# Kernel optimization log

Measured on AMD Instinct MI355X. Metric: run time of the kernel, lower is better.

## Reference

```python
import jax, jax.numpy as jnp
import numpy as np

B, S, IN, E, H, NH = 32, 1024, 16, 128, 256, 4
DH = E // NH
EPS = 1e-5


def _ln(x, g, b):
    mu = jnp.mean(x, axis=-1, keepdims=True)
    var = jnp.mean(jnp.square(x - mu), axis=-1, keepdims=True)
    return (x - mu) * jax.lax.rsqrt(var + EPS) * g + b


def setup_inputs() -> dict:
    key = jax.random.key(0)
    ks = iter(jax.random.split(key, 32))
    n = lambda shape, s=0.02: jax.random.normal(next(ks), shape, jnp.float32) * s
    inp = {
        "x": jax.random.normal(next(ks), (B, S, IN), jnp.float32),
        "mask": jax.random.uniform(next(ks), (B, S), jnp.float32),
        "embed_w": n((E, IN)), "embed_b": jnp.zeros((E,), jnp.float32),
        # 3 encoder layers, params stacked on leading layer axis
        "in_proj_w": n((3, 3 * E, E)), "in_proj_b": jnp.zeros((3, 3 * E), jnp.float32),
        "out_w": n((3, E, E)), "out_b": jnp.zeros((3, E), jnp.float32),
        "ln1_g": jnp.ones((3, E), jnp.float32), "ln1_b": jnp.zeros((3, E), jnp.float32),
        "ln2_g": jnp.ones((3, E), jnp.float32), "ln2_b": jnp.zeros((3, E), jnp.float32),
        "ffn_w1": n((3, E, E)), "ffn_b1": jnp.zeros((3, E), jnp.float32),
        "ffn_w2": n((3, E, E)), "ffn_b2": jnp.zeros((3, E), jnp.float32),
        "cls_w1": n((H, E)), "cls_b1": jnp.zeros((H,), jnp.float32),
        "cls_w2": n((H, H)), "cls_b2": jnp.zeros((H,), jnp.float32),
        "cls_w3": n((H, H)), "cls_b3": jnp.zeros((H,), jnp.float32),
        "cls_w4": n((1, H)), "cls_b4": jnp.zeros((1,), jnp.float32),
    }
    return inp


def _encoder_layer(x, ipw, ipb, ow, ob, g1, b1, g2, b2, w1, fb1, w2, fb2):
    # PyTorch TransformerEncoderLayer, norm_first=False (post-norm), relu FFN
    qkv = x @ ipw.T + ipb                      # [B,S,3E]
    q, k, v = jnp.split(qkv, 3, axis=-1)
    q = q.reshape(B, S, NH, DH).transpose(0, 2, 1, 3)
    k = k.reshape(B, S, NH, DH).transpose(0, 2, 1, 3)
    v = v.reshape(B, S, NH, DH).transpose(0, 2, 1, 3)
    scores = jnp.einsum("bhqd,bhkd->bhqk", q, k) / np.sqrt(DH)  # naive O(S^2) math SDPA
    attn = jax.nn.softmax(scores, axis=-1)
    o = jnp.einsum("bhqk,bhkd->bhqd", attn, v)
    o = o.transpose(0, 2, 1, 3).reshape(B, S, E) @ ow.T + ob
    x = _ln(x + o, g1, b1)
    ff = jax.nn.relu(x @ w1.T + fb1) @ w2.T + fb2
    return _ln(x + ff, g2, b2)


def reference(x, mask, embed_w, embed_b, in_proj_w, in_proj_b, out_w, out_b,
              ln1_g, ln1_b, ln2_g, ln2_b, ffn_w1, ffn_b1, ffn_w2, ffn_b2,
              cls_w1, cls_b1, cls_w2, cls_b2, cls_w3, cls_b3, cls_w4, cls_b4):
    h = jax.nn.relu(x @ embed_w.T + embed_b)   # [B,S,E]
    for i in range(3):
        h = _encoder_layer(h, in_proj_w[i], in_proj_b[i], out_w[i], out_b[i],
                           ln1_g[i], ln1_b[i], ln2_g[i], ln2_b[i],
                           ffn_w1[i], ffn_b1[i], ffn_w2[i], ffn_b2[i])
    pooled = jnp.sum(h * mask[:, :, None], axis=1)  # [B,E] masked sum pool
    z = jax.nn.relu(pooled @ cls_w1.T + cls_b1)
    z = jax.nn.relu(z @ cls_w2.T + cls_b2)
    z = jax.nn.relu(z @ cls_w3.T + cls_b3)
    return jax.nn.sigmoid(z @ cls_w4.T + cls_b4)    # [B,1]
```

## Files before the change

### kernel.cpp

```cpp
#include <hip/hip_runtime.h>
#include <hip/hip_bf16.h>
#include <math.h>

#define B 32
#define S 1024
#define IN_DIM 16
#define E 128
#define NH 4
#define DH 32
#define HDIM 256
#define ROWS (B*S)
#define EPS 1e-5f

#define N_IPW (3*384*128)
#define N_SQ  (3*128*128)

typedef __bf16 bf16x8 __attribute__((ext_vector_type(8)));
typedef __bf16 bf16x4 __attribute__((ext_vector_type(4)));
typedef __bf16 bf16x2 __attribute__((ext_vector_type(2)));
typedef float f32x4 __attribute__((ext_vector_type(4)));

union BF2U { bf16x2 b; unsigned int u; };
__device__ inline unsigned int pk2(float a, float b) {
    BF2U x; x.b[0] = (__bf16)a; x.b[1] = (__bf16)b; return x.u;
}

union U8 { bf16x8 v8; bf16x4 v4[2]; };
__device__ inline void st8(__bf16* p, bf16x8 v) {
    U8 u; u.v8 = v;
    *(bf16x4*)p = u.v4[0];
    *(bf16x4*)(p + 4) = u.v4[1];
}
__device__ inline bf16x8 ld8(const __bf16* p) {
    U8 u;
    u.v4[0] = *(const bf16x4*)p;
    u.v4[1] = *(const bf16x4*)(p + 4);
    return u.v8;
}

__global__ __launch_bounds__(256) void k_cvt(const float* __restrict__ ipw,
        const float* __restrict__ ow, const float* __restrict__ w1,
        const float* __restrict__ w2, __bf16* __restrict__ o)
{
    int i = blockIdx.x * 256 + threadIdx.x;
    float v;
    if (i < N_IPW) v = ipw[i];
    else if (i < N_IPW + N_SQ) v = ow[i - N_IPW];
    else if (i < N_IPW + 2 * N_SQ) v = w1[i - N_IPW - N_SQ];
    else v = w2[i - N_IPW - 2 * N_SQ];
    o[i] = (__bf16)v;
}

__global__ __launch_bounds__(128) void k_embed(const float* __restrict__ x,
        const float* __restrict__ W, const float* __restrict__ bias,
        __bf16* __restrict__ hb)
{
    int row0 = blockIdx.x * 8;
    int t = threadIdx.x;
    __shared__ float xs[8][16];
    xs[t >> 4][t & 15] = x[(row0 + (t >> 4)) * IN_DIM + (t & 15)];
    __syncthreads();
    float w[16];
#pragma unroll
    for (int i = 0; i < 16; ++i) w[i] = W[t * 16 + i];
    float bb = bias[t];
#pragma unroll
    for (int rr = 0; rr < 8; ++rr) {
        float acc = bb;
#pragma unroll
        for (int i = 0; i < 16; ++i) acc += xs[rr][i] * w[i];
        hb[(size_t)(row0 + rr) * E + t] = (__bf16)fmaxf(acc, 0.f);
    }
}

__global__ __launch_bounds__(256) void k_gemm_qkv(const __bf16* __restrict__ A,
        const __bf16* __restrict__ W, const float* __restrict__ bias,
        __bf16* __restrict__ qk, __bf16* __restrict__ vt)
{
    __shared__ __attribute__((aligned(16))) __bf16 As[128][132];
    __shared__ __attribute__((aligned(16))) __bf16 Ws[64][132];
    int t = threadIdx.x;
    int m0 = blockIdx.y * 128, n0 = blockIdx.x * 64;
    {
        int arow = t >> 1, acol = (t & 1) * 64;
        const __bf16* Ap = A + (size_t)(m0 + arow) * 128 + acol;
#pragma unroll
        for (int j = 0; j < 8; ++j)
            st8(&As[arow][acol + j * 8], *(const bf16x8*)&Ap[j * 8]);
        int wrow = t >> 2, wcol = (t & 3) * 32;
        const __bf16* Wp = W + (size_t)(n0 + wrow) * 128 + wcol;
#pragma unroll
        for (int j = 0; j < 4; ++j)
            st8(&Ws[wrow][wcol + j * 8], *(const bf16x8*)&Wp[j * 8]);
    }
    __syncthreads();
    int lane = t & 63, wv = t >> 6;
    int l15 = lane & 15, quad = lane >> 4;
    int wm = (wv & 1) * 64, wn = (wv >> 1) * 32;
    f32x4 acc[2][4];
#pragma unroll
    for (int i = 0; i < 2; ++i)
#pragma unroll
        for (int j = 0; j < 4; ++j) acc[i][j] = (f32x4){0.f, 0.f, 0.f, 0.f};
#pragma unroll
    for (int kc = 0; kc < 4; ++kc) {
        bf16x8 aw[2], ba[4];
#pragma unroll
        for (int nc = 0; nc < 2; ++nc)
            aw[nc] = ld8(&Ws[wn + nc * 16 + l15][kc * 32 + quad * 8]);
#pragma unroll
        for (int mc = 0; mc < 4; ++mc)
            ba[mc] = ld8(&As[wm + mc * 16 + l15][kc * 32 + quad * 8]);
#pragma unroll
        for (int nc = 0; nc < 2; ++nc)
#pragma unroll
            for (int mc = 0; mc < 4; ++mc)
                acc[nc][mc] = __builtin_amdgcn_mfma_f32_16x16x32_bf16(aw[nc], ba[mc], acc[nc][mc], 0, 0, 0);
    }
#pragma unroll
    for (int nc = 0; nc < 2; ++nc) {
        float4 bv = *(const float4*)&bias[n0 + wn + nc * 16 + quad * 4];
#pragma unroll
        for (int mc = 0; mc < 4; ++mc) {
            float v0 = acc[nc][mc][0] + bv.x;
            float v1 = acc[nc][mc][1] + bv.y;
            float v2 = acc[nc][mc][2] + bv.z;
            float v3 = acc[nc][mc][3] + bv.w;
            int n = n0 + wn + nc * 16 + quad * 4;
            int m = m0 + wm + mc * 16 + l15;
            if (n < 256) {
                uint2 u; u.x = pk2(v0, v1); u.y = pk2(v2, v3);
                *(uint2*)&qk[(size_t)m * 256 + n] = u;
            } else {
                int dp = n - 256;
                int hq = dp >> 5, d0 = dp & 31;
                __bf16* vp = vt + (((size_t)(m >> 10) * 4 + hq) * 32 + d0) * 1024 + (m & 1023);
                vp[0] = (__bf16)v0; vp[1024] = (__bf16)v1;
                vp[2048] = (__bf16)v2; vp[3072] = (__bf16)v3;
            }
        }
    }
}

__global__ __launch_bounds__(256) void k_gemm_ln(const __bf16* __restrict__ A,
        const __bf16* __restrict__ W, const float* __restrict__ bias,
        const float* __restrict__ g, const float* __restrict__ bta,
        __bf16* __restrict__ hb)
{
    __shared__ __attribute__((aligned(16))) __bf16 As[64][132];
    __shared__ __attribute__((aligned(16))) __bf16 Ws[128][132];
    __shared__ float red[2][64][2];
    int t = threadIdx.x;
    int m0 = blockIdx.x * 64;
    {
        int arow = t >> 2, acol = (t & 3) * 32;
        const __bf16* Ap = A + (size_t)(m0 + arow) * 128 + acol;
#pragma unroll
        for (int j = 0; j < 4; ++j)
            st8(&As[arow][acol + j * 8], *(const bf16x8*)&Ap[j * 8]);
        int wrow = t >> 1, wcol = (t & 1) * 64;
        const __bf16* Wp = W + (size_t)wrow * 128 + wcol;
#pragma unroll
        for (int j = 0; j < 8; ++j)
            st8(&Ws[wrow][wcol + j * 8], *(const bf16x8*)&Wp[j * 8]);
    }
    __syncthreads();
    int lane = t & 63, wv = t >> 6;
    int l15 = lane & 15, quad = lane >> 4;
    int nh = wv & 1, mh = wv >> 1;
    f32x4 acc[4][2];
#pragma unroll
    for (int i = 0; i < 4; ++i)
#pragma unroll
        for (int j = 0; j < 2; ++j) acc[i][j] = (f32x4){0.f, 0.f, 0.f, 0.f};
#pragma unroll
    for (int kc = 0; kc < 4; ++kc) {
        bf16x8 aw[4], ba[2];
#pragma unroll
        for (int nc = 0; nc < 4; ++nc)
            aw[nc] = ld8(&Ws[nh * 64 + nc * 16 + l15][kc * 32 + quad * 8]);
#pragma unroll
        for (int mc = 0; mc < 2; ++mc)
            ba[mc] = ld8(&As[mh * 32 + mc * 16 + l15][kc * 32 + quad * 8]);
#pragma unroll
        for (int nc = 0; nc < 4; ++nc)
#pragma unroll
            for (int mc = 0; mc < 2; ++mc)
                acc[nc][mc] = __builtin_amdgcn_mfma_f32_16x16x32_bf16(aw[nc], ba[mc], acc[nc][mc], 0, 0, 0);
    }
    float s1[2] = {0.f, 0.f}, s2[2] = {0.f, 0.f};
#pragma unroll
    for (int nc = 0; nc < 4; ++nc) {
        float4 bv = *(const float4*)&bias[nh * 64 + nc * 16 + quad * 4];
#pragma unroll
        for (int mc = 0; mc < 2; ++mc) {
            int m = m0 + mh * 32 + mc * 16 + l15;
            bf16x4 rv = *(const bf16x4*)&hb[(size_t)m * 128 + nh * 64 + nc * 16 + quad * 4];
            acc[nc][mc][0] += bv.x + (float)rv[0];
            acc[nc][mc][1] += bv.y + (float)rv[1];
            acc[nc][mc][2] += bv.z + (float)rv[2];
            acc[nc][mc][3] += bv.w + (float)rv[3];
#pragma unroll
            for (int i = 0; i < 4; ++i) {
                s1[mc] += acc[nc][mc][i];
                s2[mc] += acc[nc][mc][i] * acc[nc][mc][i];
            }
        }
    }
#pragma unroll
    for (int mc = 0; mc < 2; ++mc) {
        s1[mc] += __shfl_xor(s1[mc], 16); s1[mc] += __shfl_xor(s1[mc], 32);
        s2[mc] += __shfl_xor(s2[mc], 16); s2[mc] += __shfl_xor(s2[mc], 32);
    }
    if (quad == 0) {
#pragma unroll
        for (int mc = 0; mc < 2; ++mc) {
            red[nh][mh * 32 + mc * 16 + l15][0] = s1[mc];
            red[nh][mh * 32 + mc * 16 + l15][1] = s2[mc];
        }
    }
    __syncthreads();
    float mu[2], rs[2];
#pragma unroll
    for (int mc = 0; mc < 2; ++mc) {
        int r = mh * 32 + mc * 16 + l15;
        float S1 = red[0][r][0] + red[1][r][0];
        float S2 = red[0][r][1] + red[1][r][1];
        mu[mc] = S1 * (1.f / 128.f);
        float var = S2 * (1.f / 128.f) - mu[mc] * mu[mc];
        rs[mc] = rsqrtf(var + EPS);
    }
#pragma unroll
    for (int nc = 0; nc < 4; ++nc) {
        float4 gv = *(const float4*)&g[nh * 64 + nc * 16 + quad * 4];
        float4 bb = *(const float4*)&bta[nh * 64 + nc * 16 + quad * 4];
#pragma unroll
        for (int mc = 0; mc < 2; ++mc) {
            int m = m0 + mh * 32 + mc * 16 + l15;
            float o0 = (acc[nc][mc][0] - mu[mc]) * rs[mc] * gv.x + bb.x;
            float o1 = (acc[nc][mc][1] - mu[mc]) * rs[mc] * gv.y + bb.y;
            float o2 = (acc[nc][mc][2] - mu[mc]) * rs[mc] * gv.z + bb.z;
            float o3 = (acc[nc][mc][3] - mu[mc]) * rs[mc] * gv.w + bb.w;
            uint2 u; u.x = pk2(o0, o1); u.y = pk2(o2, o3);
            *(uint2*)&hb[(size_t)m * 128 + nh * 64 + nc * 16 + quad * 4] = u;
        }
    }
}

__global__ __launch_bounds__(256) void k_ffn(const __bf16* __restrict__ hbin,
        const __bf16* __restrict__ W1, const float* __restrict__ b1,
        const __bf16* __restrict__ W2, const float* __restrict__ b2,
        const float* __restrict__ g, const float* __restrict__ bta,
        __bf16* __restrict__ hb)
{
    __shared__ __attribute__((aligned(16))) __bf16 As[64][132];
    __shared__ __attribute__((aligned(16))) __bf16 Ws[128][132];
    __shared__ float red[2][64][2];
    int t = threadIdx.x;
    int m0 = blockIdx.x * 64;
    int arow = t >> 2, acol = (t & 3) * 32;
    int wrow = t >> 1, wcol = (t & 1) * 64;
    {
        const __bf16* Ap = hbin + (size_t)(m0 + arow) * 128 + acol;
#pragma unroll
        for (int j = 0; j < 4; ++j)
            st8(&As[arow][acol + j * 8], *(const bf16x8*)&Ap[j * 8]);
        const __bf16* Wp = W1 + (size_t)wrow * 128 + wcol;
#pragma unroll
        for (int j = 0; j < 8; ++j)
            st8(&Ws[wrow][wcol + j * 8], *(const bf16x8*)&Wp[j * 8]);
    }
    __syncthreads();
    int lane = t & 63, wv = t >> 6;
    int l15 = lane & 15, quad = lane >> 4;
    int nh = wv & 1, mh = wv >> 1;
    f32x4 acc[4][2];
#pragma unroll
    for (int i = 0; i < 4; ++i)
#pragma unroll
        for (int j = 0; j < 2; ++j) acc[i][j] = (f32x4){0.f, 0.f, 0.f, 0.f};
#pragma unroll
    for (int kc = 0; kc < 4; ++kc) {
        bf16x8 aw[4], ba[2];
#pragma unroll
        for (int nc = 0; nc < 4; ++nc)
            aw[nc] = ld8(&Ws[nh * 64 + nc * 16 + l15][kc * 32 + quad * 8]);
#pragma unroll
        for (int mc = 0; mc < 2; ++mc)
            ba[mc] = ld8(&As[mh * 32 + mc * 16 + l15][kc * 32 + quad * 8]);
#pragma unroll
        for (int nc = 0; nc < 4; ++nc)
#pragma unroll
            for (int mc = 0; mc < 2; ++mc)
                acc[nc][mc] = __builtin_amdgcn_mfma_f32_16x16x32_bf16(aw[nc], ba[mc], acc[nc][mc], 0, 0, 0);
    }
    __syncthreads();
    bf16x4 res[4][2];
#pragma unroll
    for (int nc = 0; nc < 4; ++nc)
#pragma unroll
        for (int mc = 0; mc < 2; ++mc)
            res[nc][mc] = *(const bf16x4*)&As[mh * 32 + mc * 16 + l15][nh * 64 + nc * 16 + quad * 4];
    __asm__ __volatile__("" ::: "memory");
#pragma unroll
    for (int nc = 0; nc < 4; ++nc) {
        float4 bv = *(const float4*)&b1[nh * 64 + nc * 16 + quad * 4];
#pragma unroll
        for (int mc = 0; mc < 2; ++mc) {
            float v0 = fmaxf(acc[nc][mc][0] + bv.x, 0.f);
            float v1 = fmaxf(acc[nc][mc][1] + bv.y, 0.f);
            float v2 = fmaxf(acc[nc][mc][2] + bv.z, 0.f);
            float v3 = fmaxf(acc[nc][mc][3] + bv.w, 0.f);
            uint2 u; u.x = pk2(v0, v1); u.y = pk2(v2, v3);
            *(uint2*)&As[mh * 32 + mc * 16 + l15][nh * 64 + nc * 16 + quad * 4] = u;
        }
    }
    {
        const __bf16* Wp = W2 + (size_t)wrow * 128 + wcol;
#pragma unroll
        for (int j = 0; j < 8; ++j)
            st8(&Ws[wrow][wcol + j * 8], *(const bf16x8*)&Wp[j * 8]);
    }
    __syncthreads();
#pragma unroll
    for (int i = 0; i < 4; ++i)
#pragma unroll
        for (int j = 0; j < 2; ++j) acc[i][j] = (f32x4){0.f, 0.f, 0.f, 0.f};
#pragma unroll
    for (int kc = 0; kc < 4; ++kc) {
        bf16x8 aw[4], ba[2];
#pragma unroll
        for (int nc = 0; nc < 4; ++nc)
            aw[nc] = ld8(&Ws[nh * 64 + nc * 16 + l15][kc * 32 + quad * 8]);
#pragma unroll
        for (int mc = 0; mc < 2; ++mc)
            ba[mc] = ld8(&As[mh * 32 + mc * 16 + l15][kc * 32 + quad * 8]);
#pragma unroll
        for (int nc = 0; nc < 4; ++nc)
#pragma unroll
            for (int mc = 0; mc < 2; ++mc)
                acc[nc][mc] = __builtin_amdgcn_mfma_f32_16x16x32_bf16(aw[nc], ba[mc], acc[nc][mc], 0, 0, 0);
    }
    float s1[2] = {0.f, 0.f}, s2[2] = {0.f, 0.f};
#pragma unroll
    for (int nc = 0; nc < 4; ++nc) {
        float4 bv = *(const float4*)&b2[nh * 64 + nc * 16 + quad * 4];
#pragma unroll
        for (int mc = 0; mc < 2; ++mc) {
            acc[nc][mc][0] += bv.x + (float)res[nc][mc][0];
            acc[nc][mc][1] += bv.y + (float)res[nc][mc][1];
            acc[nc][mc][2] += bv.z + (float)res[nc][mc][2];
            acc[nc][mc][3] += bv.w + (float)res[nc][mc][3];
#pragma unroll
            for (int i = 0; i < 4; ++i) {
                s1[mc] += acc[nc][mc][i];
                s2[mc] += acc[nc][mc][i] * acc[nc][mc][i];
            }
        }
    }
#pragma unroll
    for (int mc = 0; mc < 2; ++mc) {
        s1[mc] += __shfl_xor(s1[mc], 16); s1[mc] += __shfl_xor(s1[mc], 32);
        s2[mc] += __shfl_xor(s2[mc], 16); s2[mc] += __shfl_xor(s2[mc], 32);
    }
    if (quad == 0) {
#pragma unroll
        for (int mc = 0; mc < 2; ++mc) {
            red[nh][mh * 32 + mc * 16 + l15][0] = s1[mc];
            red[nh][mh * 32 + mc * 16 + l15][1] = s2[mc];
        }
    }
    __syncthreads();
    float mu[2], rs[2];
#pragma unroll
    for (int mc = 0; mc < 2; ++mc) {
        int r = mh * 32 + mc * 16 + l15;
        float S1 = red[0][r][0] + red[1][r][0];
        float S2 = red[0][r][1] + red[1][r][1];
        mu[mc] = S1 * (1.f / 128.f);
        float var = S2 * (1.f / 128.f) - mu[mc] * mu[mc];
        rs[mc] = rsqrtf(var + EPS);
    }
#pragma unroll
    for (int nc = 0; nc < 4; ++nc) {
        float4 gv = *(const float4*)&g[nh * 64 + nc * 16 + quad * 4];
        float4 bb = *(const float4*)&bta[nh * 64 + nc * 16 + quad * 4];
#pragma unroll
        for (int mc = 0; mc < 2; ++mc) {
            int m = m0 + mh * 32 + mc * 16 + l15;
            float o0 = (acc[nc][mc][0] - mu[mc]) * rs[mc] * gv.x + bb.x;
            float o1 = (acc[nc][mc][1] - mu[mc]) * rs[mc] * gv.y + bb.y;
            float o2 = (acc[nc][mc][2] - mu[mc]) * rs[mc] * gv.z + bb.z;
            float o3 = (acc[nc][mc][3] - mu[mc]) * rs[mc] * gv.w + bb.w;
            uint2 u; u.x = pk2(o0, o1); u.y = pk2(o2, o3);
            *(uint2*)&hb[(size_t)m * 128 + nh * 64 + nc * 16 + quad * 4] = u;
        }
    }
}

__global__ __launch_bounds__(256) void k_attn3(const __bf16* __restrict__ qk,
        const __bf16* __restrict__ vt, __bf16* __restrict__ O)
{
    int qt = blockIdx.x & 7, bh = blockIdx.x >> 3;
    int hh = bh & 3, b = bh >> 2;
    __shared__ __attribute__((aligned(16))) __bf16 Kb[2][64][36];
    __shared__ __attribute__((aligned(16))) __bf16 Vb[2][32][68];
    __shared__ __attribute__((aligned(16))) __bf16 Pm[4][16][68];
    int t = threadIdx.x, lane = t & 63, wv = t >> 6;
    int l15 = lane & 15, quad = lane >> 4;
    const __bf16* qbase = qk + (size_t)(b * S) * 256 + hh * 32;
    const __bf16* kbase = qk + (size_t)(b * S) * 256 + 128 + hh * 32;
    const __bf16* vbase = vt + ((size_t)(b * 4 + hh) * 32) * 1024;
    const float qscale = 0.1767766952966369f * 1.4426950408889634f;

    bf16x8 bQ[2];
#pragma unroll
    for (int gq = 0; gq < 2; ++gq) {
        bf16x8 qv = *(const bf16x8*)&qbase[(size_t)(qt * 128 + gq * 64 + wv * 16 + l15) * 256 + quad * 8];
#pragma unroll
        for (int j = 0; j < 8; ++j) bQ[gq][j] = (__bf16)((float)qv[j] * qscale);
    }

    int ksr = t >> 2, ksc = (t & 3) * 8;
    int vsr = t >> 3, vsc = (t & 7) * 8;

    {
        bf16x8 k0 = *(const bf16x8*)&kbase[(size_t)ksr * 256 + ksc];
        bf16x8 v0 = *(const bf16x8*)&vbase[(size_t)vsr * 1024 + vsc];
        st8(&Kb[0][ksr][ksc], k0);
        st8(&Vb[0][vsr][vsc], v0);
    }
    __syncthreads();

    float l_acc[2] = {0.f, 0.f};
    f32x4 o[2][2];
#pragma unroll
    for (int gq = 0; gq < 2; ++gq)
#pragma unroll
        for (int j = 0; j < 2; ++j) o[gq][j] = (f32x4){0.f, 0.f, 0.f, 0.f};

    for (int it = 0; it < 16; ++it) {
        const int cur = it & 1;
        bf16x8 knext, vnext;
        if (it < 15) {
            knext = *(const bf16x8*)&kbase[(size_t)((it + 1) * 64 + ksr) * 256 + ksc];
            vnext = *(const bf16x8*)&vbase[(size_t)vsr * 1024 + (it + 1) * 64 + vsc];
        }
        bf16x8 aK[4];
#pragma unroll
        for (int c = 0; c < 4; ++c)
            aK[c] = ld8(&Kb[cur][c * 16 + l15][quad * 8]);
        bf16x8 bv[2][2];
#pragma unroll
        for (int kc = 0; kc < 2; ++kc) {
            bv[kc][0] = ld8(&Vb[cur][l15][kc * 32 + quad * 8]);
            bv[kc][1] = ld8(&Vb[cur][16 + l15][kc * 32 + quad * 8]);
        }
#pragma unroll
        for (int gq = 0; gq < 2; ++gq) {
            f32x4 sf[4];
#pragma unroll
            for (int c = 0; c < 4; ++c)
                sf[c] = __builtin_amdgcn_mfma_f32_16x16x32_bf16(aK[c], bQ[gq], (f32x4){0.f, 0.f, 0.f, 0.f}, 0, 0, 0);
#pragma unroll
            for (int c = 0; c < 4; ++c) {
                float p0 = __builtin_amdgcn_exp2f(sf[c][0]);
                float p1 = __builtin_amdgcn_exp2f(sf[c][1]);
                float p2 = __builtin_amdgcn_exp2f(sf[c][2]);
                float p3 = __builtin_amdgcn_exp2f(sf[c][3]);
                l_acc[gq] += (p0 + p1) + (p2 + p3);
                uint2 u; u.x = pk2(p0, p1); u.y = pk2(p2, p3);
                *(uint2*)&Pm[wv][l15][c * 16 + quad * 4] = u;
            }
            __asm__ __volatile__("" ::: "memory");
#pragma unroll
            for (int kc = 0; kc < 2; ++kc) {
                bf16x8 ap = ld8(&Pm[wv][l15][kc * 32 + quad * 8]);
                o[gq][0] = __builtin_amdgcn_mfma_f32_16x16x32_bf16(ap, bv[kc][0], o[gq][0], 0, 0, 0);
                o[gq][1] = __builtin_amdgcn_mfma_f32_16x16x32_bf16(ap, bv[kc][1], o[gq][1], 0, 0, 0);
            }
            __asm__ __volatile__("" ::: "memory");
        }
        if (it < 15) {
            st8(&Kb[cur ^ 1][ksr][ksc], knext);
            st8(&Vb[cur ^ 1][vsr][vsc], vnext);
            __syncthreads();
        }
    }

#pragma unroll
    for (int gq = 0; gq < 2; ++gq) {
        float la = l_acc[gq];
        la += __shfl_xor(la, 16);
        la += __shfl_xor(la, 32);
#pragma unroll
        for (int reg = 0; reg < 4; ++reg) {
            int qloc = quad * 4 + reg;
            float linv = 1.f / __shfl(la, qloc);
            int row = qt * 128 + gq * 64 + wv * 16 + qloc;
            __bf16* op = O + ((size_t)(b * S) + row) * E + hh * 32;
            op[l15] = (__bf16)(o[gq][0][reg] * linv);
            op[16 + l15] = (__bf16)(o[gq][1][reg] * linv);
        }
    }
}

__global__ __launch_bounds__(128) void k_pool1(const __bf16* __restrict__ h,
        const float* __restrict__ mask, float* __restrict__ part)
{
    int bx = blockIdx.x;
    int b = bx >> 3, ch = bx & 7, t = threadIdx.x;
    float acc = 0.f;
    const __bf16* hp = h + (size_t)(b * S + ch * 128) * E + t;
    const float* mp = mask + b * S + ch * 128;
    for (int s = 0; s < 128; ++s) acc += (float)hp[(size_t)s * E] * mp[s];
    part[(size_t)bx * E + t] = acc;
}

__global__ __launch_bounds__(256) void k_head(const float* __restrict__ part,
        const float* __restrict__ cw1, const float* __restrict__ cb1,
        const float* __restrict__ cw2, const float* __restrict__ cb2,
        const float* __restrict__ cw3, const float* __restrict__ cb3,
        const float* __restrict__ cw4, const float* __restrict__ cb4,
        float* __restrict__ out)
{
    int b = blockIdx.x, t = threadIdx.x;
    __shared__ float p[128], za[256], zb[256];
    __shared__ float red4[4];
    if (t < 128) {
        float a = 0.f;
#pragma unroll
        for (int c = 0; c < 8; ++c) a += part[(size_t)(b * 8 + c) * 128 + t];
        p[t] = a;
    }
    __syncthreads();
    float a1 = cb1[t];
    for (int k = 0; k < 128; ++k) a1 += p[k] * cw1[t * 128 + k];
    za[t] = fmaxf(a1, 0.f);
    __syncthreads();
    float a2 = cb2[t];
    for (int k = 0; k < 256; ++k) a2 += za[k] * cw2[t * 256 + k];
    zb[t] = fmaxf(a2, 0.f);
    __syncthreads();
    float a3 = cb3[t];
    for (int k = 0; k < 256; ++k) a3 += zb[k] * cw3[t * 256 + k];
    float z3 = fmaxf(a3, 0.f);
    float prt = z3 * cw4[t];
#pragma unroll
    for (int o2 = 32; o2; o2 >>= 1) prt += __shfl_xor(prt, o2);
    if ((t & 63) == 0) red4[t >> 6] = prt;
    __syncthreads();
    if (t == 0) {
        float sum = red4[0] + red4[1] + red4[2] + red4[3] + cb4[0];
        out[b] = 1.f / (1.f + __expf(-sum));
    }
}

extern "C" void kernel_launch(void* const* d_in, const int* in_sizes, int n_in,
                              void* d_out, int out_size, void* d_ws, size_t ws_size,
                              hipStream_t stream)
{
    const float* x     = (const float*)d_in[0];
    const float* mask  = (const float*)d_in[1];
    const float* emb_w = (const float*)d_in[2];
    const float* emb_b = (const float*)d_in[3];
    const float* ipw   = (const float*)d_in[4];
    const float* ipb   = (const float*)d_in[5];
    const float* ow    = (const float*)d_in[6];
    const float* ob    = (const float*)d_in[7];
    const float* ln1g  = (const float*)d_in[8];
    const float* ln1b  = (const float*)d_in[9];
    const float* ln2g  = (const float*)d_in[10];
    const float* ln2b  = (const float*)d_in[11];
    const float* w1    = (const float*)d_in[12];
    const float* fb1   = (const float*)d_in[13];
    const float* w2    = (const float*)d_in[14];
    const float* fb2   = (const float*)d_in[15];
    const float* cw1   = (const float*)d_in[16];
    const float* cb1   = (const float*)d_in[17];
    const float* cw2   = (const float*)d_in[18];
    const float* cb2   = (const float*)d_in[19];
    const float* cw3   = (const float*)d_in[20];
    const float* cb3   = (const float*)d_in[21];
    const float* cw4   = (const float*)d_in[22];
    const float* cb4   = (const float*)d_in[23];

    char* p = (char*)d_ws;
    __bf16* hb   = (__bf16*)p;   p += (size_t)ROWS * E * 2;
    __bf16* qkb  = (__bf16*)p;   p += (size_t)ROWS * 256 * 2;
    __bf16* vtb  = (__bf16*)p;   p += (size_t)ROWS * 32 * 4 * 2 / 4;
    __bf16* t0b  = (__bf16*)p;   p += (size_t)ROWS * E * 2;
    __bf16* wb   = (__bf16*)p;   p += (size_t)(N_IPW + 3 * N_SQ) * 2;
    float* part  = (float*)p;    p += (size_t)B * 8 * E * 4;

    __bf16* wb_ipw = wb;
    __bf16* wb_ow  = wb + N_IPW;
    __bf16* wb_w1  = wb_ow + N_SQ;
    __bf16* wb_w2  = wb_w1 + N_SQ;

    k_cvt<<<(N_IPW + 3 * N_SQ) / 256, 256, 0, stream>>>(ipw, ow, w1, w2, wb);
    k_embed<<<ROWS / 8, 128, 0, stream>>>(x, emb_w, emb_b, hb);
    for (int L = 0; L < 3; ++L) {
        k_gemm_qkv<<<dim3(6, ROWS / 128), 256, 0, stream>>>(
            hb, wb_ipw + (size_t)L * 384 * 128, ipb + L * 384, qkb, vtb);
        k_attn3<<<B * NH * (S / 128), 256, 0, stream>>>(qkb, vtb, t0b);
        k_gemm_ln<<<ROWS / 64, 256, 0, stream>>>(
            t0b, wb_ow + (size_t)L * 128 * 128, ob + L * 128,
            ln1g + L * E, ln1b + L * E, hb);
        k_ffn<<<ROWS / 64, 256, 0, stream>>>(
            hb, wb_w1 + (size_t)L * 128 * 128, fb1 + L * 128,
            wb_w2 + (size_t)L * 128 * 128, fb2 + L * 128,
            ln2g + L * E, ln2b + L * E, hb);
    }
    k_pool1<<<B * 8, 128, 0, stream>>>(hb, mask, part);
    k_head<<<B, 256, 0, stream>>>(part, cw1, cb1, cw2, cb2, cw3, cb3, cw4, cb4,
                                  (float*)d_out);
}
```

Measured before the change: 342.5 us.

## Fuse out-proj+LN1 with FFN+LN2 and merge weight conversion with embedding

Combines the attention output projection with its residual LayerNorm and the two-GEMM FFN with the second LayerNorm into one kernel per 64-row tile. The LN1 result stays in shared memory and registers instead of going out to global memory and being read back. The weight bf16 conversion and the input embedding now run in a single launch, with the embedding using 16 rows per block. This cuts the launches per layer and the hb round trip, at the cost of a longer kernel that may hold more registers.

```diff
diff --git a/kernel.cpp b/kernel.cpp
--- a/kernel.cpp
+++ b/kernel.cpp
@@ -14,6 +14,7 @@
 
 #define N_IPW (3*384*128)
 #define N_SQ  (3*128*128)
+#define NCVT ((N_IPW + 3*N_SQ) / 256)
 
 typedef __bf16 bf16x8 __attribute__((ext_vector_type(8)));
 typedef __bf16 bf16x4 __attribute__((ext_vector_type(4)));
@@ -38,38 +39,40 @@
     return u.v8;
 }
 
-__global__ __launch_bounds__(256) void k_cvt(const float* __restrict__ ipw,
-        const float* __restrict__ ow, const float* __restrict__ w1,
-        const float* __restrict__ w2, __bf16* __restrict__ o)
-{
-    int i = blockIdx.x * 256 + threadIdx.x;
-    float v;
-    if (i < N_IPW) v = ipw[i];
-    else if (i < N_IPW + N_SQ) v = ow[i - N_IPW];
-    else if (i < N_IPW + 2 * N_SQ) v = w1[i - N_IPW - N_SQ];
-    else v = w2[i - N_IPW - 2 * N_SQ];
-    o[i] = (__bf16)v;
-}
-
-__global__ __launch_bounds__(128) void k_embed(const float* __restrict__ x,
-        const float* __restrict__ W, const float* __restrict__ bias,
-        __bf16* __restrict__ hb)
-{
-    int row0 = blockIdx.x * 8;
+__global__ __launch_bounds__(256) void k_embedcvt(
+        const float* __restrict__ ipw, const float* __restrict__ ow,
+        const float* __restrict__ w1, const float* __restrict__ w2,
+        __bf16* __restrict__ wbo,
+        const float* __restrict__ x, const float* __restrict__ W,
+        const float* __restrict__ bias, __bf16* __restrict__ hb)
+{
     int t = threadIdx.x;
-    __shared__ float xs[8][16];
+    if (blockIdx.x < NCVT) {
+        int i = blockIdx.x * 256 + t;
+        float v;
+        if (i < N_IPW) v = ipw[i];
+        else if (i < N_IPW + N_SQ) v = ow[i - N_IPW];
+        else if (i < N_IPW + 2 * N_SQ) v = w1[i - N_IPW - N_SQ];
+        else v = w2[i - N_IPW - 2 * N_SQ];
+        wbo[i] = (__bf16)v;
+        return;
+    }
+    int row0 = (blockIdx.x - NCVT) * 16;
+    __shared__ float xs[16][16];
     xs[t >> 4][t & 15] = x[(row0 + (t >> 4)) * IN_DIM + (t & 15)];
     __syncthreads();
+    int sub = t >> 7, tc = t & 127;
     float w[16];
 #pragma unroll
-    for (int i = 0; i < 16; ++i) w[i] = W[t * 16 + i];
-    float bb = bias[t];
+    for (int i = 0; i < 16; ++i) w[i] = W[tc * 16 + i];
+    float bb = bias[tc];
 #pragma unroll
     for (int rr = 0; rr < 8; ++rr) {
+        int lr = sub * 8 + rr;
         float acc = bb;
 #pragma unroll
-        for (int i = 0; i < 16; ++i) acc += xs[rr][i] * w[i];
-        hb[(size_t)(row0 + rr) * E + t] = (__bf16)fmaxf(acc, 0.f);
+        for (int i = 0; i < 16; ++i) acc += xs[lr][i] * w[i];
+        hb[(size_t)(row0 + lr) * E + tc] = (__bf16)fmaxf(acc, 0.f);
     }
 }
 
@@ -142,262 +145,6 @@
     }
 }
 
-__global__ __launch_bounds__(256) void k_gemm_ln(const __bf16* __restrict__ A,
-        const __bf16* __restrict__ W, const float* __restrict__ bias,
-        const float* __restrict__ g, const float* __restrict__ bta,
-        __bf16* __restrict__ hb)
-{
-    __shared__ __attribute__((aligned(16))) __bf16 As[64][132];
-    __shared__ __attribute__((aligned(16))) __bf16 Ws[128][132];
-    __shared__ float red[2][64][2];
-    int t = threadIdx.x;
-    int m0 = blockIdx.x * 64;
-    {
-        int arow = t >> 2, acol = (t & 3) * 32;
-        const __bf16* Ap = A + (size_t)(m0 + arow) * 128 + acol;
-#pragma unroll
-        for (int j = 0; j < 4; ++j)
-            st8(&As[arow][acol + j * 8], *(const bf16x8*)&Ap[j * 8]);
-        int wrow = t >> 1, wcol = (t & 1) * 64;
-        const __bf16* Wp = W + (size_t)wrow * 128 + wcol;
-#pragma unroll
-        for (int j = 0; j < 8; ++j)
-            st8(&Ws[wrow][wcol + j * 8], *(const bf16x8*)&Wp[j * 8]);
-    }
-    __syncthreads();
-    int lane = t & 63, wv = t >> 6;
-    int l15 = lane & 15, quad = lane >> 4;
-    int nh = wv & 1, mh = wv >> 1;
-    f32x4 acc[4][2];
-#pragma unroll
-    for (int i = 0; i < 4; ++i)
-#pragma unroll
-        for (int j = 0; j < 2; ++j) acc[i][j] = (f32x4){0.f, 0.f, 0.f, 0.f};
-#pragma unroll
-    for (int kc = 0; kc < 4; ++kc) {
-        bf16x8 aw[4], ba[2];
-#pragma unroll
-        for (int nc = 0; nc < 4; ++nc)
-            aw[nc] = ld8(&Ws[nh * 64 + nc * 16 + l15][kc * 32 + quad * 8]);
-#pragma unroll
-        for (int mc = 0; mc < 2; ++mc)
-            ba[mc] = ld8(&As[mh * 32 + mc * 16 + l15][kc * 32 + quad * 8]);
-#pragma unroll
-        for (int nc = 0; nc < 4; ++nc)
-#pragma unroll
-            for (int mc = 0; mc < 2; ++mc)
-                acc[nc][mc] = __builtin_amdgcn_mfma_f32_16x16x32_bf16(aw[nc], ba[mc], acc[nc][mc], 0, 0, 0);
-    }
-    float s1[2] = {0.f, 0.f}, s2[2] = {0.f, 0.f};
-#pragma unroll
-    for (int nc = 0; nc < 4; ++nc) {
-        float4 bv = *(const float4*)&bias[nh * 64 + nc * 16 + quad * 4];
-#pragma unroll
-        for (int mc = 0; mc < 2; ++mc) {
-            int m = m0 + mh * 32 + mc * 16 + l15;
-            bf16x4 rv = *(const bf16x4*)&hb[(size_t)m * 128 + nh * 64 + nc * 16 + quad * 4];
-            acc[nc][mc][0] += bv.x + (float)rv[0];
-            acc[nc][mc][1] += bv.y + (float)rv[1];
-            acc[nc][mc][2] += bv.z + (float)rv[2];
-            acc[nc][mc][3] += bv.w + (float)rv[3];
-#pragma unroll
-            for (int i = 0; i < 4; ++i) {
-                s1[mc] += acc[nc][mc][i];
-                s2[mc] += acc[nc][mc][i] * acc[nc][mc][i];
-            }
-        }
-    }
-#pragma unroll
-    for (int mc = 0; mc < 2; ++mc) {
-        s1[mc] += __shfl_xor(s1[mc], 16); s1[mc] += __shfl_xor(s1[mc], 32);
-        s2[mc] += __shfl_xor(s2[mc], 16); s2[mc] += __shfl_xor(s2[mc], 32);
-    }
-    if (quad == 0) {
-#pragma unroll
-        for (int mc = 0; mc < 2; ++mc) {
-            red[nh][mh * 32 + mc * 16 + l15][0] = s1[mc];
-            red[nh][mh * 32 + mc * 16 + l15][1] = s2[mc];
-        }
-    }
-    __syncthreads();
-    float mu[2], rs[2];
-#pragma unroll
-    for (int mc = 0; mc < 2; ++mc) {
-        int r = mh * 32 + mc * 16 + l15;
-        float S1 = red[0][r][0] + red[1][r][0];
-        float S2 = red[0][r][1] + red[1][r][1];
-        mu[mc] = S1 * (1.f / 128.f);
-        float var = S2 * (1.f / 128.f) - mu[mc] * mu[mc];
-        rs[mc] = rsqrtf(var + EPS);
-    }
-#pragma unroll
-    for (int nc = 0; nc < 4; ++nc) {
-        float4 gv = *(const float4*)&g[nh * 64 + nc * 16 + quad * 4];
-        float4 bb = *(const float4*)&bta[nh * 64 + nc * 16 + quad * 4];
-#pragma unroll
-        for (int mc = 0; mc < 2; ++mc) {
-            int m = m0 + mh * 32 + mc * 16 + l15;
-            float o0 = (acc[nc][mc][0] - mu[mc]) * rs[mc] * gv.x + bb.x;
-            float o1 = (acc[nc][mc][1] - mu[mc]) * rs[mc] * gv.y + bb.y;
-            float o2 = (acc[nc][mc][2] - mu[mc]) * rs[mc] * gv.z + bb.z;
-            float o3 = (acc[nc][mc][3] - mu[mc]) * rs[mc] * gv.w + bb.w;
-            uint2 u; u.x = pk2(o0, o1); u.y = pk2(o2, o3);
-            *(uint2*)&hb[(size_t)m * 128 + nh * 64 + nc * 16 + quad * 4] = u;
-        }
-    }
-}
-
-__global__ __launch_bounds__(256) void k_ffn(const __bf16* __restrict__ hbin,
-        const __bf16* __restrict__ W1, const float* __restrict__ b1,
-        const __bf16* __restrict__ W2, const float* __restrict__ b2,
-        const float* __restrict__ g, const float* __restrict__ bta,
-        __bf16* __restrict__ hb)
-{
-    __shared__ __attribute__((aligned(16))) __bf16 As[64][132];
-    __shared__ __attribute__((aligned(16))) __bf16 Ws[128][132];
-    __shared__ float red[2][64][2];
-    int t = threadIdx.x;
-    int m0 = blockIdx.x * 64;
-    int arow = t >> 2, acol = (t & 3) * 32;
-    int wrow = t >> 1, wcol = (t & 1) * 64;
-    {
-        const __bf16* Ap = hbin + (size_t)(m0 + arow) * 128 + acol;
-#pragma unroll
-        for (int j = 0; j < 4; ++j)
-            st8(&As[arow][acol + j * 8], *(const bf16x8*)&Ap[j * 8]);
-        const __bf16* Wp = W1 + (size_t)wrow * 128 + wcol;
-#pragma unroll
-        for (int j = 0; j < 8; ++j)
-            st8(&Ws[wrow][wcol + j * 8], *(const bf16x8*)&Wp[j * 8]);
-    }
-    __syncthreads();
-    int lane = t & 63, wv = t >> 6;
-    int l15 = lane & 15, quad = lane >> 4;
-    int nh = wv & 1, mh = wv >> 1;
-    f32x4 acc[4][2];
-#pragma unroll
-    for (int i = 0; i < 4; ++i)
-#pragma unroll
-        for (int j = 0; j < 2; ++j) acc[i][j] = (f32x4){0.f, 0.f, 0.f, 0.f};
-#pragma unroll
-    for (int kc = 0; kc < 4; ++kc) {
-        bf16x8 aw[4], ba[2];
-#pragma unroll
-        for (int nc = 0; nc < 4; ++nc)
-            aw[nc] = ld8(&Ws[nh * 64 + nc * 16 + l15][kc * 32 + quad * 8]);
-#pragma unroll
-        for (int mc = 0; mc < 2; ++mc)
-            ba[mc] = ld8(&As[mh * 32 + mc * 16 + l15][kc * 32 + quad * 8]);
-#pragma unroll
-        for (int nc = 0; nc < 4; ++nc)
-#pragma unroll
-            for (int mc = 0; mc < 2; ++mc)
-                acc[nc][mc] = __builtin_amdgcn_mfma_f32_16x16x32_bf16(aw[nc], ba[mc], acc[nc][mc], 0, 0, 0);
-    }
-    __syncthreads();
-    bf16x4 res[4][2];
-#pragma unroll
-    for (int nc = 0; nc < 4; ++nc)
-#pragma unroll
-        for (int mc = 0; mc < 2; ++mc)
-            res[nc][mc] = *(const bf16x4*)&As[mh * 32 + mc * 16 + l15][nh * 64 + nc * 16 + quad * 4];
-    __asm__ __volatile__("" ::: "memory");
-#pragma unroll
-    for (int nc = 0; nc < 4; ++nc) {
-        float4 bv = *(const float4*)&b1[nh * 64 + nc * 16 + quad * 4];
-#pragma unroll
-        for (int mc = 0; mc < 2; ++mc) {
-            float v0 = fmaxf(acc[nc][mc][0] + bv.x, 0.f);
-            float v1 = fmaxf(acc[nc][mc][1] + bv.y, 0.f);
-            float v2 = fmaxf(acc[nc][mc][2] + bv.z, 0.f);
-            float v3 = fmaxf(acc[nc][mc][3] + bv.w, 0.f);
-            uint2 u; u.x = pk2(v0, v1); u.y = pk2(v2, v3);
-            *(uint2*)&As[mh * 32 + mc * 16 + l15][nh * 64 + nc * 16 + quad * 4] = u;
-        }
-    }
-    {
-        const __bf16* Wp = W2 + (size_t)wrow * 128 + wcol;
-#pragma unroll
-        for (int j = 0; j < 8; ++j)
-            st8(&Ws[wrow][wcol + j * 8], *(const bf16x8*)&Wp[j * 8]);
-    }
-    __syncthreads();
-#pragma unroll
-    for (int i = 0; i < 4; ++i)
-#pragma unroll
-        for (int j = 0; j < 2; ++j) acc[i][j] = (f32x4){0.f, 0.f, 0.f, 0.f};
-#pragma unroll
-    for (int kc = 0; kc < 4; ++kc) {
-        bf16x8 aw[4], ba[2];
-#pragma unroll
-        for (int nc = 0; nc < 4; ++nc)
-            aw[nc] = ld8(&Ws[nh * 64 + nc * 16 + l15][kc * 32 + quad * 8]);
-#pragma unroll
-        for (int mc = 0; mc < 2; ++mc)
-            ba[mc] = ld8(&As[mh * 32 + mc * 16 + l15][kc * 32 + quad * 8]);
-#pragma unroll
-        for (int nc = 0; nc < 4; ++nc)
-#pragma unroll
-            for (int mc = 0; mc < 2; ++mc)
-                acc[nc][mc] = __builtin_amdgcn_mfma_f32_16x16x32_bf16(aw[nc], ba[mc], acc[nc][mc], 0, 0, 0);
-    }
-    float s1[2] = {0.f, 0.f}, s2[2] = {0.f, 0.f};
-#pragma unroll
-    for (int nc = 0; nc < 4; ++nc) {
-        float4 bv = *(const float4*)&b2[nh * 64 + nc * 16 + quad * 4];
-#pragma unroll
-        for (int mc = 0; mc < 2; ++mc) {
-            acc[nc][mc][0] += bv.x + (float)res[nc][mc][0];
-            acc[nc][mc][1] += bv.y + (float)res[nc][mc][1];
-            acc[nc][mc][2] += bv.z + (float)res[nc][mc][2];
-            acc[nc][mc][3] += bv.w + (float)res[nc][mc][3];
-#pragma unroll
-            for (int i = 0; i < 4; ++i) {
-                s1[mc] += acc[nc][mc][i];
-                s2[mc] += acc[nc][mc][i] * acc[nc][mc][i];
-            }
-        }
-    }
-#pragma unroll
-    for (int mc = 0; mc < 2; ++mc) {
-        s1[mc] += __shfl_xor(s1[mc], 16); s1[mc] += __shfl_xor(s1[mc], 32);
-        s2[mc] += __shfl_xor(s2[mc], 16); s2[mc] += __shfl_xor(s2[mc], 32);
-    }
-    if (quad == 0) {
-#pragma unroll
-        for (int mc = 0; mc < 2; ++mc) {
-            red[nh][mh * 32 + mc * 16 + l15][0] = s1[mc];
-            red[nh][mh * 32 + mc * 16 + l15][1] = s2[mc];
-        }
-    }
-    __syncthreads();
-    float mu[2], rs[2];
-#pragma unroll
-    for (int mc = 0; mc < 2; ++mc) {
-        int r = mh * 32 + mc * 16 + l15;
-        float S1 = red[0][r][0] + red[1][r][0];
-        float S2 = red[0][r][1] + red[1][r][1];
-        mu[mc] = S1 * (1.f / 128.f);
-        float var = S2 * (1.f / 128.f) - mu[mc] * mu[mc];
-        rs[mc] = rsqrtf(var + EPS);
-    }
-#pragma unroll
-    for (int nc = 0; nc < 4; ++nc) {
-        float4 gv = *(const float4*)&g[nh * 64 + nc * 16 + quad * 4];
-        float4 bb = *(const float4*)&bta[nh * 64 + nc * 16 + quad * 4];
-#pragma unroll
-        for (int mc = 0; mc < 2; ++mc) {
-            int m = m0 + mh * 32 + mc * 16 + l15;
-            float o0 = (acc[nc][mc][0] - mu[mc]) * rs[mc] * gv.x + bb.x;
-            float o1 = (acc[nc][mc][1] - mu[mc]) * rs[mc] * gv.y + bb.y;
-            float o2 = (acc[nc][mc][2] - mu[mc]) * rs[mc] * gv.z + bb.z;
-            float o3 = (acc[nc][mc][3] - mu[mc]) * rs[mc] * gv.w + bb.w;
-            uint2 u; u.x = pk2(o0, o1); u.y = pk2(o2, o3);
-            *(uint2*)&hb[(size_t)m * 128 + nh * 64 + nc * 16 + quad * 4] = u;
-        }
-    }
-}
-
 __global__ __launch_bounds__(256) void k_attn3(const __bf16* __restrict__ qk,
         const __bf16* __restrict__ vt, __bf16* __restrict__ O)
 {
@@ -501,6 +248,240 @@
             __bf16* op = O + ((size_t)(b * S) + row) * E + hh * 32;
             op[l15] = (__bf16)(o[gq][0][reg] * linv);
             op[16 + l15] = (__bf16)(o[gq][1][reg] * linv);
+        }
+    }
+}
+
+__global__ __launch_bounds__(256) void k_layer2(const __bf16* __restrict__ t0b,
+        const __bf16* __restrict__ Wo, const float* __restrict__ ob,
+        const float* __restrict__ g1, const float* __restrict__ bt1,
+        const __bf16* __restrict__ W1, const float* __restrict__ b1v,
+        const __bf16* __restrict__ W2, const float* __restrict__ b2v,
+        const float* __restrict__ g2, const float* __restrict__ bt2,
+        __bf16* __restrict__ hb)
+{
+    __shared__ __attribute__((aligned(16))) __bf16 As[64][132];
+    __shared__ __attribute__((aligned(16))) __bf16 Ws[128][132];
+    __shared__ float red[2][64][2];
+    int t = threadIdx.x;
+    int m0 = blockIdx.x * 64;
+    int arow = t >> 2, acol = (t & 3) * 32;
+    int wrow = t >> 1, wcol = (t & 1) * 64;
+    {
+        const __bf16* Ap = t0b + (size_t)(m0 + arow) * 128 + acol;
+#pragma unroll
+        for (int j = 0; j < 4; ++j)
+            st8(&As[arow][acol + j * 8], *(const bf16x8*)&Ap[j * 8]);
+        const __bf16* Wp = Wo + (size_t)wrow * 128 + wcol;
+#pragma unroll
+        for (int j = 0; j < 8; ++j)
+            st8(&Ws[wrow][wcol + j * 8], *(const bf16x8*)&Wp[j * 8]);
+    }
+    __syncthreads();
+    int lane = t & 63, wv = t >> 6;
+    int l15 = lane & 15, quad = lane >> 4;
+    int nh = wv & 1, mh = wv >> 1;
+    f32x4 acc[4][2];
+
+#pragma unroll
+    for (int i = 0; i < 4; ++i)
+#pragma unroll
+        for (int j = 0; j < 2; ++j) acc[i][j] = (f32x4){0.f, 0.f, 0.f, 0.f};
+#pragma unroll
+    for (int kc = 0; kc < 4; ++kc) {
+        bf16x8 aw[4], ba[2];
+#pragma unroll
+        for (int nc = 0; nc < 4; ++nc)
+            aw[nc] = ld8(&Ws[nh * 64 + nc * 16 + l15][kc * 32 + quad * 8]);
+#pragma unroll
+        for (int mc = 0; mc < 2; ++mc)
+            ba[mc] = ld8(&As[mh * 32 + mc * 16 + l15][kc * 32 + quad * 8]);
+#pragma unroll
+        for (int nc = 0; nc < 4; ++nc)
+#pragma unroll
+            for (int mc = 0; mc < 2; ++mc)
+                acc[nc][mc] = __builtin_amdgcn_mfma_f32_16x16x32_bf16(aw[nc], ba[mc], acc[nc][mc], 0, 0, 0);
+    }
+    float s1[2] = {0.f, 0.f}, s2[2] = {0.f, 0.f};
+#pragma unroll
+    for (int nc = 0; nc < 4; ++nc) {
+        float4 bv = *(const float4*)&ob[nh * 64 + nc * 16 + quad * 4];
+#pragma unroll
+        for (int mc = 0; mc < 2; ++mc) {
+            int m = m0 + mh * 32 + mc * 16 + l15;
+            bf16x4 rv = *(const bf16x4*)&hb[(size_t)m * 128 + nh * 64 + nc * 16 + quad * 4];
+            acc[nc][mc][0] += bv.x + (float)rv[0];
+            acc[nc][mc][1] += bv.y + (float)rv[1];
+            acc[nc][mc][2] += bv.z + (float)rv[2];
+            acc[nc][mc][3] += bv.w + (float)rv[3];
+#pragma unroll
+            for (int i = 0; i < 4; ++i) {
+                s1[mc] += acc[nc][mc][i];
+                s2[mc] += acc[nc][mc][i] * acc[nc][mc][i];
+            }
+        }
+    }
+#pragma unroll
+    for (int mc = 0; mc < 2; ++mc) {
+        s1[mc] += __shfl_xor(s1[mc], 16); s1[mc] += __shfl_xor(s1[mc], 32);
+        s2[mc] += __shfl_xor(s2[mc], 16); s2[mc] += __shfl_xor(s2[mc], 32);
+    }
+    if (quad == 0) {
+#pragma unroll
+        for (int mc = 0; mc < 2; ++mc) {
+            red[nh][mh * 32 + mc * 16 + l15][0] = s1[mc];
+            red[nh][mh * 32 + mc * 16 + l15][1] = s2[mc];
+        }
+    }
+    __syncthreads();
+    float mu[2], rs[2];
+#pragma unroll
+    for (int mc = 0; mc < 2; ++mc) {
+        int r = mh * 32 + mc * 16 + l15;
+        float S1 = red[0][r][0] + red[1][r][0];
+        float S2 = red[0][r][1] + red[1][r][1];
+        mu[mc] = S1 * (1.f / 128.f);
+        float var = S2 * (1.f / 128.f) - mu[mc] * mu[mc];
+        rs[mc] = rsqrtf(var + EPS);
+    }
+    bf16x4 res2[4][2];
+#pragma unroll
+    for (int nc = 0; nc < 4; ++nc) {
+        float4 gv = *(const float4*)&g1[nh * 64 + nc * 16 + quad * 4];
+        float4 bb = *(const float4*)&bt1[nh * 64 + nc * 16 + quad * 4];
+#pragma unroll
+        for (int mc = 0; mc < 2; ++mc) {
+            float o0 = (acc[nc][mc][0] - mu[mc]) * rs[mc] * gv.x + bb.x;
+            float o1 = (acc[nc][mc][1] - mu[mc]) * rs[mc] * gv.y + bb.y;
+            float o2 = (acc[nc][mc][2] - mu[mc]) * rs[mc] * gv.z + bb.z;
+            float o3 = (acc[nc][mc][3] - mu[mc]) * rs[mc] * gv.w + bb.w;
+            bf16x4 xb;
+            xb[0] = (__bf16)o0; xb[1] = (__bf16)o1;
+            xb[2] = (__bf16)o2; xb[3] = (__bf16)o3;
+            res2[nc][mc] = xb;
+            *(bf16x4*)&As[mh * 32 + mc * 16 + l15][nh * 64 + nc * 16 + quad * 4] = xb;
+        }
+    }
+    {
+        const __bf16* Wp = W1 + (size_t)wrow * 128 + wcol;
+#pragma unroll
+        for (int j = 0; j < 8; ++j)
+            st8(&Ws[wrow][wcol + j * 8], *(const bf16x8*)&Wp[j * 8]);
+    }
+    __syncthreads();
+
+#pragma unroll
+    for (int i = 0; i < 4; ++i)
+#pragma unroll
+        for (int j = 0; j < 2; ++j) acc[i][j] = (f32x4){0.f, 0.f, 0.f, 0.f};
+#pragma unroll
+    for (int kc = 0; kc < 4; ++kc) {
+        bf16x8 aw[4], ba[2];
+#pragma unroll
+        for (int nc = 0; nc < 4; ++nc)
+            aw[nc] = ld8(&Ws[nh * 64 + nc * 16 + l15][kc * 32 + quad * 8]);
+#pragma unroll
+        for (int mc = 0; mc < 2; ++mc)
+            ba[mc] = ld8(&As[mh * 32 + mc * 16 + l15][kc * 32 + quad * 8]);
+#pragma unroll
+        for (int nc = 0; nc < 4; ++nc)
+#pragma unroll
+            for (int mc = 0; mc < 2; ++mc)
+                acc[nc][mc] = __builtin_amdgcn_mfma_f32_16x16x32_bf16(aw[nc], ba[mc], acc[nc][mc], 0, 0, 0);
+    }
+    __syncthreads();
+#pragma unroll
+    for (int nc = 0; nc < 4; ++nc) {
+        float4 bv = *(const float4*)&b1v[nh * 64 + nc * 16 + quad * 4];
+#pragma unroll
+        for (int mc = 0; mc < 2; ++mc) {
+            float v0 = fmaxf(acc[nc][mc][0] + bv.x, 0.f);
+            float v1 = fmaxf(acc[nc][mc][1] + bv.y, 0.f);
+            float v2 = fmaxf(acc[nc][mc][2] + bv.z, 0.f);
+            float v3 = fmaxf(acc[nc][mc][3] + bv.w, 0.f);
+            uint2 u; u.x = pk2(v0, v1); u.y = pk2(v2, v3);
+            *(uint2*)&As[mh * 32 + mc * 16 + l15][nh * 64 + nc * 16 + quad * 4] = u;
+        }
+    }
+    {
+        const __bf16* Wp = W2 + (size_t)wrow * 128 + wcol;
+#pragma unroll
+        for (int j = 0; j < 8; ++j)
+            st8(&Ws[wrow][wcol + j * 8], *(const bf16x8*)&Wp[j * 8]);
+    }
+    __syncthreads();
+
+#pragma unroll
+    for (int i = 0; i < 4; ++i)
+#pragma unroll
+        for (int j = 0; j < 2; ++j) acc[i][j] = (f32x4){0.f, 0.f, 0.f, 0.f};
+#pragma unroll
+    for (int kc = 0; kc < 4; ++kc) {
+        bf16x8 aw[4], ba[2];
+#pragma unroll
+        for (int nc = 0; nc < 4; ++nc)
+            aw[nc] = ld8(&Ws[nh * 64 + nc * 16 + l15][kc * 32 + quad * 8]);
+#pragma unroll
+        for (int mc = 0; mc < 2; ++mc)
+            ba[mc] = ld8(&As[mh * 32 + mc * 16 + l15][kc * 32 + quad * 8]);
+#pragma unroll
+        for (int nc = 0; nc < 4; ++nc)
+#pragma unroll
+            for (int mc = 0; mc < 2; ++mc)
+                acc[nc][mc] = __builtin_amdgcn_mfma_f32_16x16x32_bf16(aw[nc], ba[mc], acc[nc][mc], 0, 0, 0);
+    }
+    s1[0] = s1[1] = s2[0] = s2[1] = 0.f;
+#pragma unroll
+    for (int nc = 0; nc < 4; ++nc) {
+        float4 bv = *(const float4*)&b2v[nh * 64 + nc * 16 + quad * 4];
+#pragma unroll
+        for (int mc = 0; mc < 2; ++mc) {
+            acc[nc][mc][0] += bv.x + (float)res2[nc][mc][0];
+            acc[nc][mc][1] += bv.y + (float)res2[nc][mc][1];
+            acc[nc][mc][2] += bv.z + (float)res2[nc][mc][2];
+            acc[nc][mc][3] += bv.w + (float)res2[nc][mc][3];
+#pragma unroll
+            for (int i = 0; i < 4; ++i) {
+                s1[mc] += acc[nc][mc][i];
+                s2[mc] += acc[nc][mc][i] * acc[nc][mc][i];
+            }
+        }
+    }
+#pragma unroll
+    for (int mc = 0; mc < 2; ++mc) {
+        s1[mc] += __shfl_xor(s1[mc], 16); s1[mc] += __shfl_xor(s1[mc], 32);
+        s2[mc] += __shfl_xor(s2[mc], 16); s2[mc] += __shfl_xor(s2[mc], 32);
+    }
+    if (quad == 0) {
+#pragma unroll
+        for (int mc = 0; mc < 2; ++mc) {
+            red[nh][mh * 32 + mc * 16 + l15][0] = s1[mc];
+            red[nh][mh * 32 + mc * 16 + l15][1] = s2[mc];
+        }
+    }
+    __syncthreads();
+#pragma unroll
+    for (int mc = 0; mc < 2; ++mc) {
+        int r = mh * 32 + mc * 16 + l15;
+        float S1 = red[0][r][0] + red[1][r][0];
+        float S2 = red[0][r][1] + red[1][r][1];
+        mu[mc] = S1 * (1.f / 128.f);
+        float var = S2 * (1.f / 128.f) - mu[mc] * mu[mc];
+        rs[mc] = rsqrtf(var + EPS);
+    }
+#pragma unroll
+    for (int nc = 0; nc < 4; ++nc) {
+        float4 gv = *(const float4*)&g2[nh * 64 + nc * 16 + quad * 4];
+        float4 bb = *(const float4*)&bt2[nh * 64 + nc * 16 + quad * 4];
+#pragma unroll
+        for (int mc = 0; mc < 2; ++mc) {
+            int m = m0 + mh * 32 + mc * 16 + l15;
+            float o0 = (acc[nc][mc][0] - mu[mc]) * rs[mc] * gv.x + bb.x;
+            float o1 = (acc[nc][mc][1] - mu[mc]) * rs[mc] * gv.y + bb.y;
+            float o2 = (acc[nc][mc][2] - mu[mc]) * rs[mc] * gv.z + bb.z;
+            float o3 = (acc[nc][mc][3] - mu[mc]) * rs[mc] * gv.w + bb.w;
+            uint2 u; u.x = pk2(o0, o1); u.y = pk2(o2, o3);
+            *(uint2*)&hb[(size_t)m * 128 + nh * 64 + nc * 16 + quad * 4] = u;
         }
     }
 }
@@ -598,17 +579,16 @@
     __bf16* wb_w1  = wb_ow + N_SQ;
     __bf16* wb_w2  = wb_w1 + N_SQ;
 
-    k_cvt<<<(N_IPW + 3 * N_SQ) / 256, 256, 0, stream>>>(ipw, ow, w1, w2, wb);
-    k_embed<<<ROWS / 8, 128, 0, stream>>>(x, emb_w, emb_b, hb);
+    k_embedcvt<<<NCVT + ROWS / 16, 256, 0, stream>>>(
+        ipw, ow, w1, w2, wb, x, emb_w, emb_b, hb);
     for (int L = 0; L < 3; ++L) {
         k_gemm_qkv<<<dim3(6, ROWS / 128), 256, 0, stream>>>(
             hb, wb_ipw + (size_t)L * 384 * 128, ipb + L * 384, qkb, vtb);
         k_attn3<<<B * NH * (S / 128), 256, 0, stream>>>(qkb, vtb, t0b);
-        k_gemm_ln<<<ROWS / 64, 256, 0, stream>>>(
+        k_layer2<<<ROWS / 64, 256, 0, stream>>>(
             t0b, wb_ow + (size_t)L * 128 * 128, ob + L * 128,
-            ln1g + L * E, ln1b + L * E, hb);
-        k_ffn<<<ROWS / 64, 256, 0, stream>>>(
-            hb, wb_w1 + (size_t)L * 128 * 128, fb1 + L * 128,
+            ln1g + L * E, ln1b + L * E,
+            wb_w1 + (size_t)L * 128 * 128, fb1 + L * 128,
             wb_w2 + (size_t)L * 128 * 128, fb2 + L * 128,
             ln2g + L * E, ln2b + L * E, hb);
     }
```

Result: no change. 336.1 us (-1.9%).
